# Performance work log

Measured on AMD Instinct MI355X. Metric: run time of the kernel, lower is better.

## Reference

```python
import jax, jax.numpy as jnp
import numpy as np

B, C, H, W = 128, 3, 512, 640  # (H//4)*(W//4) = 20480 = encoder in_features
D_ENC, D_ATT = 128, 32


def setup_inputs() -> dict:
    key = jax.random.key(0)
    ks = jax.random.split(key, 12)
    s = lambda k, shape, sc: jax.random.normal(k, shape, jnp.float32) * sc
    return {
        "f1_norm": jax.random.normal(ks[0], (B, C, H, W), jnp.float32),
        "f2_norm": jax.random.normal(ks[1], (B, H, W), jnp.float32),
        # torch Linear convention: weight shape (out_features, in_features)
        "W1": s(ks[2], (D_ENC, 20480), 0.007), "b1": jnp.zeros((D_ENC,), jnp.float32),
        "W2": s(ks[3], (D_ENC, 20480), 0.007), "b2": jnp.zeros((D_ENC,), jnp.float32),
        "Aa": s(ks[4], (3, 3), 0.5), "Av": s(ks[5], (3, 3), 0.5),
        "Wa": s(ks[6], (D_ATT, 3), 0.5), "Wv": s(ks[7], (D_ATT, 3), 0.5),
        "Wca": s(ks[8], (D_ATT, 2 * D_ENC), 0.06), "Wcv": s(ks[9], (D_ATT, 2 * D_ENC), 0.06),
        "Wha": s(ks[10], (3, D_ATT), 0.18), "Whv": s(ks[11], (3, D_ATT), 0.18),
    }


def reference(f1_norm, f2_norm, W1, b1, W2, b2, Aa, Av, Wa, Wv, Wca, Wcv, Wha, Whv):
    b = f1_norm.shape[0]
    # F.interpolate(scale_factor=1/4, mode='nearest') == strided slice by 4
    a = f1_norm[:, :, ::4, ::4].reshape(b, 3, -1)      # (B,3,20480)
    v = f2_norm[:, ::4, ::4].reshape(b, 1, -1)
    v = jnp.concatenate([v, v, v], axis=1)             # (B,3,20480)

    aud = jnp.einsum('bcd,kd->bck', a, W1) + b1        # (B,3,128) encoder1
    vis = jnp.einsum('bcd,kd->bck', v, W2) + b2        # (B,3,128) encoder2
    av = jnp.concatenate([aud, vis], axis=2)           # (B,3,256)

    scale = 1.0 / jnp.sqrt(jnp.float32(2 * D_ENC))     # 1/sqrt(256)
    # a_t = affine_a(av^T); att_aud = aud^T @ a_t^T = aud^T @ (Aa @ av)
    Aav = jnp.einsum('ij,bjm->bim', Aa, av)            # (B,3,256)
    audio_att = jnp.tanh(jnp.einsum('bik,bim->bkm', aud, Aav) * scale)  # (B,128,256)
    Vav = jnp.einsum('ij,bjm->bim', Av, av)
    vis_att = jnp.tanh(jnp.einsum('bik,bim->bkm', vis, Vav) * scale)    # (B,128,256)

    H_a = jax.nn.relu(jnp.einsum('bkm,hm->bkh', audio_att, Wca)
                      + jnp.einsum('bik,hi->bkh', aud, Wa))             # (B,128,32)
    H_v = jax.nn.relu(jnp.einsum('bkm,hm->bkh', vis_att, Wcv)
                      + jnp.einsum('bik,hi->bkh', vis, Wv))

    att_audio = jnp.einsum('bkh,ch->bck', H_a, Wha) + aud               # (B,3,128)
    att_visual = jnp.einsum('bkh,ch->bck', H_v, Whv) + vis              # (B,3,128)
    return jnp.concatenate([att_audio, att_visual], axis=2)             # (B,3,256)
```

## Files before the change

### kernel.cpp

```cpp
#include <hip/hip_runtime.h>

constexpr int KDIM   = 20480;
constexpr int MAUD   = 384;
constexpr int MTOT   = 512;
constexpr int DENC   = 128;
constexpr int SPLIT  = 64;
constexpr int KCHUNK = KDIM / SPLIT;
constexpr int BK     = 64;
constexpr int MTILE  = 64;
constexpr int LDA    = 72;
constexpr int LDB    = 72;

typedef __bf16 bf16_t;
typedef __bf16 v8bf __attribute__((ext_vector_type(8)));
typedef float  v4f  __attribute__((ext_vector_type(4)));

static __device__ inline unsigned short f2bf(float x) {
    union { float f; unsigned u; } a; a.f = x;
    unsigned r = a.u + 0x7FFFu + ((a.u >> 16) & 1u);
    return (unsigned short)(r >> 16);
}

static __device__ inline float tanh_fast(float x) {
    float e = __expf(2.f * x);
    return 1.f - 2.f * __builtin_amdgcn_rcpf(e + 1.f);
}

__global__ __launch_bounds__(256) void gemm_stage1(
    const float* __restrict__ f1, const float* __restrict__ f2,
    const float* __restrict__ W1, const float* __restrict__ W2,
    float* __restrict__ P)
{
    __shared__ bf16_t lA[MTILE * LDA];
    __shared__ bf16_t lB[DENC * LDB];

    const int bx    = blockIdx.x;
    const int mtile = bx >> 6;
    const int s     = bx & 63;
    const int t     = threadIdx.x;

    const int arow = t >> 2;
    const int kseg = (t & 3) * 16;
    const int r    = mtile * MTILE + arow;
    const float* abase = (r < MAUD) ? (f1 + (size_t)r * 327680)
                                    : (f2 + (size_t)(r - MAUD) * 327680);
    const int bn  = t >> 1;
    const int bk0 = (t & 1) * 32;
    const float* wrow = ((mtile < 6) ? W1 : W2) + (size_t)bn * KDIM;

    const int wave = t >> 6, lane = t & 63;
    const int wr  = wave >> 1, wc = wave & 1;
    const int l15 = lane & 15, lq = lane >> 4;

    v4f acc[2][4];
#pragma unroll
    for (int a = 0; a < 2; ++a)
#pragma unroll
        for (int b = 0; b < 4; ++b) acc[a][b] = (v4f)0.f;

    for (int bk = 0; bk < KCHUNK / BK; ++bk) {
        const int kc = s * KCHUNK + bk * BK;
        {
            int d = kc + kseg;
            int i = d / 160, j = d - i * 160;
#pragma unroll
            for (int g = 0; g < 2; ++g) {
                unsigned pk[4];
#pragma unroll
                for (int q = 0; q < 4; ++q) {
                    float v0 = abase[i * 2560 + j * 4];
                    j++; if (j == 160) { j = 0; i++; }
                    float v1 = abase[i * 2560 + j * 4];
                    j++; if (j == 160) { j = 0; i++; }
                    pk[q] = (unsigned)f2bf(v0) | ((unsigned)f2bf(v1) << 16);
                }
                *(uint4*)&lA[arow * LDA + kseg + g * 8] =
                    make_uint4(pk[0], pk[1], pk[2], pk[3]);
            }
        }
        {
            const float4* wp = (const float4*)(wrow + kc + bk0);
#pragma unroll
            for (int g = 0; g < 4; ++g) {
                float4 x = wp[g * 2];
                float4 y = wp[g * 2 + 1];
                uint4 pk;
                pk.x = (unsigned)f2bf(x.x) | ((unsigned)f2bf(x.y) << 16);
                pk.y = (unsigned)f2bf(x.z) | ((unsigned)f2bf(x.w) << 16);
                pk.z = (unsigned)f2bf(y.x) | ((unsigned)f2bf(y.y) << 16);
                pk.w = (unsigned)f2bf(y.z) | ((unsigned)f2bf(y.w) << 16);
                *(uint4*)&lB[bn * LDB + bk0 + g * 8] = pk;
            }
        }
        __syncthreads();
#pragma unroll
        for (int kk = 0; kk < 2; ++kk) {
            const int kl = kk * 32 + lq * 8;
            v8bf fa[2], fb[4];
#pragma unroll
            for (int mi = 0; mi < 2; ++mi)
                fa[mi] = *(const v8bf*)&lA[(wr * 32 + mi * 16 + l15) * LDA + kl];
#pragma unroll
            for (int ni = 0; ni < 4; ++ni)
                fb[ni] = *(const v8bf*)&lB[(wc * 64 + ni * 16 + l15) * LDB + kl];
#pragma unroll
            for (int mi = 0; mi < 2; ++mi)
#pragma unroll
                for (int ni = 0; ni < 4; ++ni)
                    acc[mi][ni] = __builtin_amdgcn_mfma_f32_16x16x32_bf16(
                        fa[mi], fb[ni], acc[mi][ni], 0, 0, 0);
        }
        __syncthreads();
    }
#pragma unroll
    for (int mi = 0; mi < 2; ++mi)
#pragma unroll
        for (int ni = 0; ni < 4; ++ni)
#pragma unroll
            for (int v = 0; v < 4; ++v) {
                int row = mtile * MTILE + wr * 32 + mi * 16 + lq * 4 + v;
                int col = wc * 64 + ni * 16 + l15;
                P[((size_t)row * SPLIT + s) * DENC + col] = acc[mi][ni][v];
            }
}

__global__ __launch_bounds__(256) void stage2(
    const float* __restrict__ P,
    const float* __restrict__ b1, const float* __restrict__ b2,
    const float* __restrict__ Aa, const float* __restrict__ Av,
    const float* __restrict__ Wa, const float* __restrict__ Wv,
    const float* __restrict__ Wca, const float* __restrict__ Wcv,
    const float* __restrict__ Wha, const float* __restrict__ Whv,
    float* __restrict__ out)
{
    __shared__ float s_aud[3][128];
    __shared__ float s_vis[128];
    __shared__ float s_M[3][256];
    __shared__ float s_Wc[32 * 256];
    __shared__ float s_H[2][128][33];

    const int gid = blockIdx.x;
    const int b   = gid >> 1;
    const int isv = gid & 1;
    const int t   = threadIdx.x;

    for (int o = t; o < 512; o += 256) {
        if (o < 384) {
            const int c = o >> 7, k = o & 127;
            float acc = b1[k];
            const float* p = P + (size_t)(3 * b + c) * SPLIT * 128 + k;
#pragma unroll 4
            for (int sp = 0; sp < SPLIT; ++sp) acc += p[sp * 128];
            s_aud[c][k] = acc;
        } else {
            const int k = o - 384;
            float acc = b2[k];
            const float* p = P + (size_t)(384 + b) * SPLIT * 128 + k;
#pragma unroll 4
            for (int sp = 0; sp < SPLIT; ++sp) acc += p[sp * 128];
            s_vis[k] = acc;
        }
    }
    {
        const float4* wg = (const float4*)(isv ? Wcv : Wca);
        float4* ws4 = (float4*)s_Wc;
        for (int idx = t; idx < 2048; idx += 256) ws4[idx] = wg[idx];
    }
    __syncthreads();

    {
        const int m = t;
        const float av0 = (m < 128) ? s_aud[0][m] : s_vis[m - 128];
        const float av1 = (m < 128) ? s_aud[1][m] : s_vis[m - 128];
        const float av2 = (m < 128) ? s_aud[2][m] : s_vis[m - 128];
        if (!isv) {
#pragma unroll
            for (int i = 0; i < 3; ++i)
                s_M[i][m] = Aa[3 * i] * av0 + Aa[3 * i + 1] * av1 + Aa[3 * i + 2] * av2;
        } else {
            const float c0 = Av[0] + Av[3] + Av[6];
            const float c1 = Av[1] + Av[4] + Av[7];
            const float c2 = Av[2] + Av[5] + Av[8];
            s_M[0][m] = c0 * av0 + c1 * av1 + c2 * av2;
        }
    }
    __syncthreads();

    {
        const int k = t & 127, half = t >> 7;
        float hacc[32];
#pragma unroll
        for (int h = 0; h < 32; ++h) hacc[h] = 0.f;
        const float scale = 0.0625f;
        const float4* M4 = (const float4*)s_M;
        const float4* W4 = (const float4*)s_Wc;
        float a0 = 0.f, a1 = 0.f, a2 = 0.f, vk = 0.f;
        if (!isv) { a0 = s_aud[0][k]; a1 = s_aud[1][k]; a2 = s_aud[2][k]; }
        else      { vk = s_vis[k]; }
        for (int cc = 0; cc < 32; ++cc) {
            const int mi = half * 32 + cc;
            const float4 m0 = M4[mi];
            float s0, s1, s2, s3;
            if (!isv) {
                const float4 m1 = M4[64 + mi], m2 = M4[128 + mi];
                s0 = scale * (a0 * m0.x + a1 * m1.x + a2 * m2.x);
                s1 = scale * (a0 * m0.y + a1 * m1.y + a2 * m2.y);
                s2 = scale * (a0 * m0.z + a1 * m1.z + a2 * m2.z);
                s3 = scale * (a0 * m0.w + a1 * m1.w + a2 * m2.w);
            } else {
                s0 = scale * vk * m0.x; s1 = scale * vk * m0.y;
                s2 = scale * vk * m0.z; s3 = scale * vk * m0.w;
            }
            const float t0 = tanh_fast(s0), t1 = tanh_fast(s1);
            const float t2 = tanh_fast(s2), t3 = tanh_fast(s3);
#pragma unroll
            for (int h = 0; h < 32; ++h) {
                const float4 w = W4[h * 64 + mi];
                hacc[h] = fmaf(t0, w.x, fmaf(t1, w.y, fmaf(t2, w.z, fmaf(t3, w.w, hacc[h]))));
            }
        }
#pragma unroll
        for (int h = 0; h < 32; ++h) s_H[half][k][h] = hacc[h];
    }
    __syncthreads();

    if (t < 128) {
        const int k = t;
        const float* Wh  = isv ? Whv : Wha;
        const float* Wab = isv ? Wv  : Wa;
        float p0, p1, p2;
        if (!isv) { p0 = s_aud[0][k]; p1 = s_aud[1][k]; p2 = s_aud[2][k]; }
        else      { p0 = p1 = p2 = s_vis[k]; }
        float o0 = 0.f, o1 = 0.f, o2 = 0.f;
#pragma unroll
        for (int h = 0; h < 32; ++h) {
            float wb = p0 * Wab[h * 3] + p1 * Wab[h * 3 + 1] + p2 * Wab[h * 3 + 2];
            float hv = s_H[0][k][h] + s_H[1][k][h] + wb;
            hv = fmaxf(hv, 0.f);
            o0 = fmaf(hv, Wh[h], o0);
            o1 = fmaf(hv, Wh[32 + h], o1);
            o2 = fmaf(hv, Wh[64 + h], o2);
        }
        const size_t ob = (size_t)b * 768 + (isv ? 128 : 0) + k;
        if (!isv) {
            out[ob]       = o0 + s_aud[0][k];
            out[ob + 256] = o1 + s_aud[1][k];
            out[ob + 512] = o2 + s_aud[2][k];
        } else {
            const float v = s_vis[k];
            out[ob]       = o0 + v;
            out[ob + 256] = o1 + v;
            out[ob + 512] = o2 + v;
        }
    }
}

extern "C" void kernel_launch(void* const* d_in, const int* in_sizes, int n_in,
                              void* d_out, int out_size, void* d_ws, size_t ws_size,
                              hipStream_t stream) {
    const float* f1  = (const float*)d_in[0];
    const float* f2  = (const float*)d_in[1];
    const float* W1  = (const float*)d_in[2];
    const float* b1  = (const float*)d_in[3];
    const float* W2  = (const float*)d_in[4];
    const float* b2  = (const float*)d_in[5];
    const float* Aa  = (const float*)d_in[6];
    const float* Av  = (const float*)d_in[7];
    const float* Wa  = (const float*)d_in[8];
    const float* Wv  = (const float*)d_in[9];
    const float* Wca = (const float*)d_in[10];
    const float* Wcv = (const float*)d_in[11];
    const float* Wha = (const float*)d_in[12];
    const float* Whv = (const float*)d_in[13];
    float* P   = (float*)d_ws;
    float* out = (float*)d_out;

    hipLaunchKernelGGL(gemm_stage1, dim3(512), dim3(256), 0, stream,
                       f1, f2, W1, W2, P);
    hipLaunchKernelGGL(stage2, dim3(256), dim3(256), 0, stream,
                       P, b1, b2, Aa, Av, Wa, Wv, Wca, Wcv, Wha, Whv, out);
}
```

Before: 716.7 us.

## Double-buffer LDS tiles with register prefetch in split-K encoder GEMM

The stage-1 GEMM loop now loads the next K-tile of strided input and weights into registers before computing on the current LDS buffer. After the MFMAs it converts that data to bf16 and writes it into a second LDS buffer, so global-load latency overlaps with compute. This also drops one __syncthreads per iteration. The strided-gather addressing is rewritten without per-element wraparound branches, and the 5-iteration loop is fully unrolled. In exchange, LDS use doubles and register pressure rises from the 16 floats plus 8 float4 held per thread.

```diff
diff --git a/kernel.cpp b/kernel.cpp
--- a/kernel.cpp
+++ b/kernel.cpp
@@ -31,8 +31,8 @@
     const float* __restrict__ W1, const float* __restrict__ W2,
     float* __restrict__ P)
 {
-    __shared__ bf16_t lA[MTILE * LDA];
-    __shared__ bf16_t lB[DENC * LDB];
+    __shared__ bf16_t lA[2][MTILE * LDA];
+    __shared__ bf16_t lB[2][DENC * LDB];
 
     const int bx    = blockIdx.x;
     const int mtile = bx >> 6;
@@ -46,7 +46,8 @@
                                     : (f2 + (size_t)(r - MAUD) * 327680);
     const int bn  = t >> 1;
     const int bk0 = (t & 1) * 32;
-    const float* wrow = ((mtile < 6) ? W1 : W2) + (size_t)bn * KDIM;
+    const float* wbase = ((mtile < 6) ? W1 : W2)
+                       + (size_t)bn * KDIM + s * KCHUNK + bk0;
 
     const int wave = t >> 6, lane = t & 63;
     const int wr  = wave >> 1, wc = wave & 1;
@@ -58,40 +59,52 @@
 #pragma unroll
         for (int b = 0; b < 4; ++b) acc[a][b] = (v4f)0.f;
 
+    float  av[16];
+    float4 bv[8];
+
+#define LOAD_TILE(bk_) do {                                                   \
+    const int db_ = s * KCHUNK + kseg + (bk_) * BK;                           \
+    const int i0_ = db_ / 160;                                                \
+    const int j0_ = db_ - i0_ * 160;                                          \
+    _Pragma("unroll")                                                         \
+    for (int e = 0; e < 16; ++e) {                                            \
+        const int i_ = i0_ + ((j0_ + e) >= 160);                              \
+        av[e] = abase[4 * (db_ + e) + 1920 * i_];                             \
+    }                                                                         \
+    const float4* wp_ = (const float4*)(wbase + (bk_) * BK);                  \
+    _Pragma("unroll")                                                         \
+    for (int g = 0; g < 8; ++g) bv[g] = wp_[g];                               \
+} while (0)
+
+#define STORE_TILE(buf_) do {                                                 \
+    unsigned pk_[8];                                                          \
+    _Pragma("unroll")                                                         \
+    for (int q = 0; q < 8; ++q)                                               \
+        pk_[q] = (unsigned)f2bf(av[2 * q]) |                                  \
+                 ((unsigned)f2bf(av[2 * q + 1]) << 16);                       \
+    *(uint4*)&lA[buf_][arow * LDA + kseg] =                                   \
+        make_uint4(pk_[0], pk_[1], pk_[2], pk_[3]);                           \
+    *(uint4*)&lA[buf_][arow * LDA + kseg + 8] =                               \
+        make_uint4(pk_[4], pk_[5], pk_[6], pk_[7]);                           \
+    _Pragma("unroll")                                                         \
+    for (int g = 0; g < 4; ++g) {                                             \
+        const float4 x_ = bv[2 * g], y_ = bv[2 * g + 1];                      \
+        uint4 w_;                                                             \
+        w_.x = (unsigned)f2bf(x_.x) | ((unsigned)f2bf(x_.y) << 16);           \
+        w_.y = (unsigned)f2bf(x_.z) | ((unsigned)f2bf(x_.w) << 16);           \
+        w_.z = (unsigned)f2bf(y_.x) | ((unsigned)f2bf(y_.y) << 16);           \
+        w_.w = (unsigned)f2bf(y_.z) | ((unsigned)f2bf(y_.w) << 16);           \
+        *(uint4*)&lB[buf_][bn * LDB + bk0 + g * 8] = w_;                      \
+    }                                                                         \
+} while (0)
+
+    LOAD_TILE(0);
+    STORE_TILE(0);
+
+    int cur = 0;
+#pragma unroll
     for (int bk = 0; bk < KCHUNK / BK; ++bk) {
-        const int kc = s * KCHUNK + bk * BK;
-        {
-            int d = kc + kseg;
-            int i = d / 160, j = d - i * 160;
-#pragma unroll
-            for (int g = 0; g < 2; ++g) {
-                unsigned pk[4];
-#pragma unroll
-                for (int q = 0; q < 4; ++q) {
-                    float v0 = abase[i * 2560 + j * 4];
-                    j++; if (j == 160) { j = 0; i++; }
-                    float v1 = abase[i * 2560 + j * 4];
-                    j++; if (j == 160) { j = 0; i++; }
-                    pk[q] = (unsigned)f2bf(v0) | ((unsigned)f2bf(v1) << 16);
-                }
-                *(uint4*)&lA[arow * LDA + kseg + g * 8] =
-                    make_uint4(pk[0], pk[1], pk[2], pk[3]);
-            }
-        }
-        {
-            const float4* wp = (const float4*)(wrow + kc + bk0);
-#pragma unroll
-            for (int g = 0; g < 4; ++g) {
-                float4 x = wp[g * 2];
-                float4 y = wp[g * 2 + 1];
-                uint4 pk;
-                pk.x = (unsigned)f2bf(x.x) | ((unsigned)f2bf(x.y) << 16);
-                pk.y = (unsigned)f2bf(x.z) | ((unsigned)f2bf(x.w) << 16);
-                pk.z = (unsigned)f2bf(y.x) | ((unsigned)f2bf(y.y) << 16);
-                pk.w = (unsigned)f2bf(y.z) | ((unsigned)f2bf(y.w) << 16);
-                *(uint4*)&lB[bn * LDB + bk0 + g * 8] = pk;
-            }
-        }
+        if (bk < KCHUNK / BK - 1) LOAD_TILE(bk + 1);
         __syncthreads();
 #pragma unroll
         for (int kk = 0; kk < 2; ++kk) {
@@ -99,10 +112,10 @@
             v8bf fa[2], fb[4];
 #pragma unroll
             for (int mi = 0; mi < 2; ++mi)
-                fa[mi] = *(const v8bf*)&lA[(wr * 32 + mi * 16 + l15) * LDA + kl];
+                fa[mi] = *(const v8bf*)&lA[cur][(wr * 32 + mi * 16 + l15) * LDA + kl];
 #pragma unroll
             for (int ni = 0; ni < 4; ++ni)
-                fb[ni] = *(const v8bf*)&lB[(wc * 64 + ni * 16 + l15) * LDB + kl];
+                fb[ni] = *(const v8bf*)&lB[cur][(wc * 64 + ni * 16 + l15) * LDB + kl];
 #pragma unroll
             for (int mi = 0; mi < 2; ++mi)
 #pragma unroll
@@ -110,8 +123,11 @@
                     acc[mi][ni] = __builtin_amdgcn_mfma_f32_16x16x32_bf16(
                         fa[mi], fb[ni], acc[mi][ni], 0, 0, 0);
         }
-        __syncthreads();
-    }
+        if (bk < KCHUNK / BK - 1) { STORE_TILE(cur ^ 1); cur ^= 1; }
+    }
+#undef LOAD_TILE
+#undef STORE_TILE
+
 #pragma unroll
     for (int mi = 0; mi < 2; ++mi)
 #pragma unroll
```

Result: no change. 715.4 us (-0.2%).
